# Kernel optimization log

Hardware: AMD Instinct MI355X
Metric: run time of the kernel (lower is better)

## Reference

```python
import math
import jax, jax.numpy as jnp
import numpy as np

N_HEAD = 16
ROPE_BASE = 10000.0


def _rope_tables(T, half, dtype):
    # build_sin_cos(seq_len, dim=head_dim//2): inv freq of length `half`
    pos = jnp.arange(T, dtype=jnp.float32)[:, None]                       # (T,1)
    inv = jnp.exp(jnp.arange(0, 2 * half, 2, dtype=jnp.float32) * (-math.log(ROPE_BASE) / (2 * half)))
    ang = pos * inv                                                        # (T, half)
    return jnp.sin(ang).astype(dtype), jnp.cos(ang).astype(dtype)


def _apply_rope(q, k, sin, cos):
    # q,k: (B,T,H,Dh); sin,cos: (T, Dh//2) -> broadcast over batch and heads
    half = q.shape[-1] // 2
    s = sin[None, :, None, :]
    c = cos[None, :, None, :]
    q1, q2 = q[..., :half], q[..., half:]
    k1, k2 = k[..., :half], k[..., half:]
    q = jnp.concatenate([q1 * c - q2 * s, q2 * c + q1 * s], axis=-1)
    k = jnp.concatenate([k1 * c - k2 * s, k2 * c + k1 * s], axis=-1)
    return q, k


def setup_inputs() -> dict:
    key = jax.random.key(0)
    k1, k2, k3 = jax.random.split(key, 3)
    B, T, C = 2, 2048, 2048
    x = jax.random.normal(k1, (B, T, C), dtype=jnp.float32)
    w_qkv = jax.random.normal(k2, (3 * C, C), dtype=jnp.float32) * (1.0 / math.sqrt(C))
    w_proj = jax.random.normal(k3, (C, C), dtype=jnp.float32) * (1.0 / math.sqrt(C))
    return {"x": x, "w_qkv": w_qkv, "w_proj": w_proj}


def reference(x, w_qkv, w_proj):
    B, T, C = x.shape
    H = N_HEAD
    Dh = C // H
    # fused QKV projection (Linear, no bias): (B,T,3C) -> (B,T,3,H,Dh)
    qkv = jnp.einsum('btc,oc->bto', x, w_qkv).reshape(B, T, 3, H, Dh)
    q, k, v = qkv[:, :, 0], qkv[:, :, 1], qkv[:, :, 2]          # (B,T,H,Dh)
    sin, cos = _rope_tables(T, Dh // 2, x.dtype)
    q, k = _apply_rope(q, k, sin, cos)
    # causal attention, scale 1/sqrt(Dh) (flash default softmax_scale=None)
    scale = 1.0 / math.sqrt(Dh)
    scores = jnp.einsum('bqhd,bkhd->bhqk', q, k) * scale        # (B,H,T,T)
    mask = jnp.tril(jnp.ones((T, T), dtype=bool))
    scores = jnp.where(mask[None, None], scores, jnp.finfo(scores.dtype).min)
    probs = jax.nn.softmax(scores, axis=-1)
    out = jnp.einsum('bhqk,bkhd->bqhd', probs, v)               # (B,T,H,Dh)
    # faithful to original: permute(0,2,1,3) then reshape_as(x)
    out = jnp.transpose(out, (0, 2, 1, 3)).reshape(B, T, C)
    return jnp.einsum('btc,oc->bto', out, w_proj)
```

## Files before the change

### kernel.cpp

```cpp
#include <hip/hip_runtime.h>
#include <hip/hip_bf16.h>

typedef __bf16 bf16_t;
typedef __bf16 bf16x8 __attribute__((ext_vector_type(8)));
typedef float f32x4 __attribute__((ext_vector_type(4)));

#define MFMA16(a, b, c) __builtin_amdgcn_mfma_f32_16x16x32_bf16(a, b, c, 0, 0, 0)

__device__ __forceinline__ void async_copy16(const void* g, void* l) {
  __builtin_amdgcn_global_load_lds(
      (const __attribute__((address_space(1))) void*)g,
      (__attribute__((address_space(3))) void*)l, 16, 0, 0);
}

__global__ void cast_f32_bf16(const float* __restrict__ in, bf16_t* __restrict__ out, int n8) {
  int stride = gridDim.x * blockDim.x;
  for (int i = blockIdx.x * blockDim.x + threadIdx.x; i < n8; i += stride) {
    const float* p = in + (size_t)i * 8;
    f32x4 a = *(const f32x4*)p;
    f32x4 b = *(const f32x4*)(p + 4);
    bf16x8 o;
    o[0] = (bf16_t)a[0]; o[1] = (bf16_t)a[1]; o[2] = (bf16_t)a[2]; o[3] = (bf16_t)a[3];
    o[4] = (bf16_t)b[0]; o[5] = (bf16_t)b[1]; o[6] = (bf16_t)b[2]; o[7] = (bf16_t)b[3];
    *(bf16x8*)(out + (size_t)i * 8) = o;
  }
}

__global__ __launch_bounds__(512, 2) void gemm_qkv(
    const bf16_t* __restrict__ A, const bf16_t* __restrict__ Bw,
    bf16_t* __restrict__ qo, bf16_t* __restrict__ ko,
    int K) {
  __shared__ __align__(16) char lds[131072];
  int tid = threadIdx.x;
  int w = tid >> 6, lane = tid & 63;
  int wm = w & 1, wn = w >> 1;
  int mr = lane & 15, kg = lane >> 4;

  int orig = blockIdx.x;
  int chunk = orig & 7, i = orig >> 3;
  int by = (chunk & 3) * 4 + (i & 3);
  int bx = (chunk >> 2) * 8 + (i >> 2);
  int row0 = by * 256, col0 = bx * 256;

  int lr = tid >> 3, ch = (tid & 7) ^ (lr & 7);
  size_t aoff[4], boff[4];
#pragma unroll
  for (int g = 0; g < 4; ++g) {
    int gr = g * 32 + (lr & 31) + (lr >> 5) * 128;
    aoff[g] = (size_t)(row0 + gr) * K + ch * 8;
  }
#pragma unroll
  for (int p = 0; p < 4; ++p) {
    int gr = (lr >> 4) * 64 + p * 16 + (lr & 15);
    boff[p] = (size_t)(col0 + gr) * K + ch * 8;
  }

  auto stgA = [&](int q, int g, int kt) {
    async_copy16(A + aoff[g] + kt * 64, lds + q * 65536 + g * 8192 + tid * 16);
  };
  auto stgB = [&](int q, int p, int kt) {
    async_copy16(Bw + boff[p] + kt * 64, lds + q * 65536 + 32768 + p * 8192 + tid * 16);
  };

  f32x4 zero = {0.f, 0.f, 0.f, 0.f};
  f32x4 acc[8][4];
#pragma unroll
  for (int mi = 0; mi < 8; ++mi)
#pragma unroll
    for (int ni = 0; ni < 4; ++ni) acc[mi][ni] = zero;

  int nt = K >> 6;

  stgB(0, 0, 0); stgB(0, 1, 0); stgB(0, 2, 0); stgB(0, 3, 0);
  stgA(0, 0, 0); stgA(0, 1, 0); stgA(0, 2, 0); stgA(0, 3, 0);
  asm volatile("s_waitcnt vmcnt(0)" ::: "memory");
  __builtin_amdgcn_sched_barrier(0);
  __builtin_amdgcn_s_barrier();
  __builtin_amdgcn_sched_barrier(0);

#pragma unroll 1
  for (int t = 0; t < nt; ++t) {
    int q = t & 1, qn = q ^ 1;
    int kt = (t + 1 < nt) ? (t + 1) : t;
    const char* Ab = lds + q * 65536;
    const char* Bb = Ab + 32768;
    bf16x8 bf[4][2];

#define QKV_PHASE(MI0, STG0, STG1, WAIT)                                        \
    {                                                                           \
      int r0 = ((MI0) >> 1) * 64 + wm * 32 + mr;                                \
      int r1 = r0 + 16;                                                         \
      bf16x8 a00 = *(const bf16x8*)(Ab + r0 * 128 + ((kg * 16) ^ ((r0 & 7) << 4)));      \
      bf16x8 a01 = *(const bf16x8*)(Ab + r0 * 128 + ((64 + kg * 16) ^ ((r0 & 7) << 4))); \
      bf16x8 a10 = *(const bf16x8*)(Ab + r1 * 128 + ((kg * 16) ^ ((r1 & 7) << 4)));      \
      bf16x8 a11 = *(const bf16x8*)(Ab + r1 * 128 + ((64 + kg * 16) ^ ((r1 & 7) << 4))); \
      STG0; STG1;                                                               \
      __builtin_amdgcn_sched_barrier(0);                                        \
      asm volatile("s_waitcnt vmcnt(" #WAIT ")" ::: "memory");                  \
      __builtin_amdgcn_s_barrier();                                             \
      asm volatile("s_waitcnt lgkmcnt(0)" ::: "memory");                        \
      __builtin_amdgcn_sched_barrier(0);                                        \
      __builtin_amdgcn_s_setprio(1);                                            \
      _Pragma("unroll")                                                         \
      for (int ni = 0; ni < 4; ++ni) {                                          \
        acc[MI0][ni] = MFMA16(a00, bf[ni][0], acc[MI0][ni]);                    \
        acc[MI0][ni] = MFMA16(a01, bf[ni][1], acc[MI0][ni]);                    \
        acc[(MI0) + 1][ni] = MFMA16(a10, bf[ni][0], acc[(MI0) + 1][ni]);        \
        acc[(MI0) + 1][ni] = MFMA16(a11, bf[ni][1], acc[(MI0) + 1][ni]);        \
      }                                                                         \
      __builtin_amdgcn_s_setprio(0);                                            \
      __builtin_amdgcn_sched_barrier(0);                                        \
      __builtin_amdgcn_s_barrier();                                             \
      __builtin_amdgcn_sched_barrier(0);                                        \
    }

#pragma unroll
    for (int ni = 0; ni < 4; ++ni) {
      int rb = ni * 64 + wn * 16 + mr;
      bf[ni][0] = *(const bf16x8*)(Bb + rb * 128 + ((kg * 16) ^ ((rb & 7) << 4)));
      bf[ni][1] = *(const bf16x8*)(Bb + rb * 128 + ((64 + kg * 16) ^ ((rb & 7) << 4)));
    }
    QKV_PHASE(0, stgB(qn, 0, kt), stgB(qn, 1, kt), 4)
    QKV_PHASE(2, stgB(qn, 2, kt), stgB(qn, 3, kt), 5)
    QKV_PHASE(4, stgA(qn, 0, kt), stgA(qn, 1, kt), 6)
    QKV_PHASE(6, stgA(qn, 2, kt), stgA(qn, 3, kt), 3)
#undef QKV_PHASE
  }
  asm volatile("s_waitcnt vmcnt(0)" ::: "memory");
  __syncthreads();

  char* tb = &lds[0];
  int s = col0 >> 11;
  int h0 = (col0 >> 7) & 15;
  int b = row0 >> 11, t0 = row0 & 2047;
#pragma unroll
  for (int mi = 0; mi < 8; ++mi)
#pragma unroll
    for (int ni = 0; ni < 4; ++ni)
#pragma unroll
      for (int jj = 0; jj < 4; ++jj) {
        int rl = wm * 128 + mi * 16 + kg * 4 + jj;
        int cb = (wn * 64 + ni * 16 + mr) * 2;
        *(bf16_t*)(tb + rl * 512 + (cb ^ ((rl & 7) << 4))) = (bf16_t)acc[mi][ni][jj];
      }
  __syncthreads();
  int r = tid >> 1, hs = tid & 1;
  const char* rowb = tb + r * 512;
  int sz = (r & 7) << 4;
  int t = t0 + r;
  bf16_t* dst = (s == 0 ? qo : ko) + ((size_t)((b * 16 + h0 + hs) * 2048 + t)) * 128;
  float tf = (float)t;
  const float cinv = -0.20762050593046014f;
  bf16x8 vin[16];
#pragma unroll
  for (int m = 0; m < 16; ++m)
    vin[m] = *(const bf16x8*)(rowb + ((hs * 256 + m * 16) ^ sz));
#pragma unroll
  for (int m = 0; m < 8; ++m) {
    bf16x8 o1, o2;
#pragma unroll
    for (int e = 0; e < 8; ++e) {
      float ang = tf * exp2f((float)(m * 8 + e) * cinv);
      float sv = __sinf(ang), cv = __cosf(ang);
      float x1 = (float)vin[m][e], x2 = (float)vin[m + 8][e];
      o1[e] = (bf16_t)(x1 * cv - x2 * sv);
      o2[e] = (bf16_t)(x2 * cv + x1 * sv);
    }
    *(bf16x8*)(dst + m * 8) = o1;
    *(bf16x8*)(dst + 64 + m * 8) = o2;
  }
}

template <int MODE>
__global__ __launch_bounds__(512, 2) void gemm256(
    const bf16_t* __restrict__ A, const bf16_t* __restrict__ Bw, float* __restrict__ C,
    bf16_t* __restrict__ vto, int M, int N, int K, int nby, int colbase) {
  __shared__ __align__(16) char lds[147456];
  int tid = threadIdx.x;
  int w = tid >> 6, lane = tid & 63;
  int wm = w >> 1, wn = w & 1;
  int mr = lane & 15, kg = lane >> 4;

  int nwg = gridDim.x;
  int orig = blockIdx.x;
  int wgid = (orig & 7) * (nwg >> 3) + (orig >> 3);
  int by = wgid % nby, bx = wgid / nby;
  int row0 = by * 256, col0 = colbase + bx * 128;

  size_t aoff[4], boff[2];
#pragma unroll
  for (int it = 0; it < 4; ++it) {
    int c = tid + it * 512;
    int r = c >> 3;
    int chs = (c & 7) ^ (r & 7);
    aoff[it] = (size_t)(row0 + r) * K + chs * 8;
  }
#pragma unroll
  for (int it = 0; it < 2; ++it) {
    int c = tid + it * 512;
    int r = c >> 3;
    int chs = (c & 7) ^ (r & 7);
    boff[it] = (size_t)(col0 - colbase + r) * K + chs * 8;
  }

  auto stageA = [&](int buf, int kt, int half) {
    char* Ad = &lds[buf * 49152];
#pragma unroll
    for (int it = half * 2; it < half * 2 + 2; ++it)
      async_copy16(A + aoff[it] + kt * 64, Ad + (tid + it * 512) * 16);
  };
  auto stageB = [&](int buf, int kt) {
    char* Bd = &lds[buf * 49152 + 32768];
#pragma unroll
    for (int it = 0; it < 2; ++it)
      async_copy16(Bw + boff[it] + kt * 64, Bd + (tid + it * 512) * 16);
  };

  f32x4 zero = {0.f, 0.f, 0.f, 0.f};
  f32x4 acc[4][4];
#pragma unroll
  for (int mi = 0; mi < 4; ++mi)
#pragma unroll
    for (int ni = 0; ni < 4; ++ni) acc[mi][ni] = zero;

  int nt = K >> 6;
  stageA(0, 0, 0); stageA(0, 0, 1); stageB(0, 0);
  stageA(1, 1, 0); stageA(1, 1, 1); stageB(1, 1);
  asm volatile("s_waitcnt vmcnt(6)" ::: "memory");
  __builtin_amdgcn_sched_barrier(0);
  __builtin_amdgcn_s_barrier();
  __builtin_amdgcn_sched_barrier(0);

#pragma unroll 1
  for (int t = 0; t < nt; ++t) {
    int cur = t % 3;
    int nxt = (t + 2) % 3;
    int kt2 = (t + 2 < nt) ? (t + 2) : t;
    const char* Ab = &lds[cur * 49152];
    const char* Bb = &lds[cur * 49152 + 32768];
    bf16x8 af[4][2], bfr[4][2];
#pragma unroll
    for (int mi = 0; mi < 4; ++mi) {
      int row = wm * 64 + mi * 16 + mr;
      const char* rb = Ab + row * 128;
      int sz = (row & 7) << 4;
      af[mi][0] = *(const bf16x8*)(rb + ((kg * 16) ^ sz));
      af[mi][1] = *(const bf16x8*)(rb + ((64 + kg * 16) ^ sz));
    }
#pragma unroll
    for (int ni = 0; ni < 4; ++ni) {
      int row = wn * 64 + ni * 16 + mr;
      const char* rb = Bb + row * 128;
      int sz = (row & 7) << 4;
      bfr[ni][0] = *(const bf16x8*)(rb + ((kg * 16) ^ sz));
      bfr[ni][1] = *(const bf16x8*)(rb + ((64 + kg * 16) ^ sz));
    }
    stageA(nxt, kt2, 0);
    __builtin_amdgcn_s_setprio(1);
#pragma unroll
    for (int mi = 0; mi < 4; ++mi) {
      acc[mi][0] = MFMA16(af[mi][0], bfr[0][0], acc[mi][0]);
      acc[mi][0] = MFMA16(af[mi][1], bfr[0][1], acc[mi][0]);
    }
    __builtin_amdgcn_s_setprio(0);
    stageA(nxt, kt2, 1);
    __builtin_amdgcn_s_setprio(1);
#pragma unroll
    for (int mi = 0; mi < 4; ++mi) {
      acc[mi][1] = MFMA16(af[mi][0], bfr[1][0], acc[mi][1]);
      acc[mi][1] = MFMA16(af[mi][1], bfr[1][1], acc[mi][1]);
    }
    __builtin_amdgcn_s_setprio(0);
    stageB(nxt, kt2);
    __builtin_amdgcn_s_setprio(1);
#pragma unroll
    for (int mi = 0; mi < 4; ++mi) {
      acc[mi][2] = MFMA16(af[mi][0], bfr[2][0], acc[mi][2]);
      acc[mi][2] = MFMA16(af[mi][1], bfr[2][1], acc[mi][2]);
      acc[mi][3] = MFMA16(af[mi][0], bfr[3][0], acc[mi][3]);
      acc[mi][3] = MFMA16(af[mi][1], bfr[3][1], acc[mi][3]);
    }
    __builtin_amdgcn_s_setprio(0);
    asm volatile("s_waitcnt vmcnt(6)" ::: "memory");
    __builtin_amdgcn_sched_barrier(0);
    __builtin_amdgcn_s_barrier();
    __builtin_amdgcn_sched_barrier(0);
  }
  asm volatile("s_waitcnt vmcnt(0)" ::: "memory");
  __syncthreads();

  if (MODE == 0) {
#pragma unroll
    for (int mi = 0; mi < 4; ++mi)
#pragma unroll
      for (int ni = 0; ni < 4; ++ni)
#pragma unroll
        for (int jj = 0; jj < 4; ++jj) {
          int row = row0 + wm * 64 + mi * 16 + kg * 4 + jj;
          int col = col0 + wn * 64 + ni * 16 + mr;
          C[(size_t)row * N + col] = acc[mi][ni][jj];
        }
  } else {
    char* tb = &lds[0];
    int h = (col0 >> 7) & 15;
    int b = row0 >> 11, t0 = row0 & 2047;
#pragma unroll
    for (int mi = 0; mi < 4; ++mi)
#pragma unroll
      for (int ni = 0; ni < 4; ++ni)
#pragma unroll
        for (int jj = 0; jj < 4; ++jj) {
          int rloc = wm * 64 + mi * 16 + kg * 4 + jj;
          int cloc = wn * 64 + ni * 16 + mr;
          *(bf16_t*)(tb + cloc * 512 + ((rloc * 2) ^ ((cloc & 7) << 4))) =
              (bf16_t)acc[mi][ni][jj];
        }
    __syncthreads();
    int d = tid >> 2, qt = tid & 3;
    const char* rowb = tb + d * 512;
    int sz = (d & 7) << 4;
    bf16_t* dst = vto + ((size_t)((b * 16 + h) * 128 + d)) * 2048 + t0 + qt * 64;
#pragma unroll
    for (int m2 = 0; m2 < 8; ++m2)
      *(bf16x8*)(dst + m2 * 8) = *(const bf16x8*)(rowb + ((qt * 128 + m2 * 16) ^ sz));
  }
}

__global__ __launch_bounds__(256) void attn_kernel(
    const bf16_t* __restrict__ qg, const bf16_t* __restrict__ kgl,
    const bf16_t* __restrict__ vtg, bf16_t* __restrict__ og) {
  __shared__ __align__(16) bf16_t Ks[2][64 * 128];
  __shared__ __align__(16) bf16_t Vs[2][128 * 64];
  __shared__ __align__(16) bf16_t plds[4][1024];
  const int T = 2048;
  int tid = threadIdx.x;
  int w = tid >> 6, lane = tid & 63;
  int mr = lane & 15, kg = lane >> 4;
  int swz = (mr & 7) << 4;

  int L = blockIdx.y * 16 + blockIdx.x;
  int role = (L & 7) * 64 + (L >> 3);
  int bx = role & 15, bh = role >> 4;

  const bf16_t* Q = qg + (size_t)bh * T * 128;
  const bf16_t* K = kgl + (size_t)bh * T * 128;
  const bf16_t* Vt = vtg + (size_t)bh * 128 * T;

  int sb = tid * 16;
  int krl = sb >> 8;
  int kc = (sb & 255) ^ ((krl & 7) << 4);
  size_t ksrc = (size_t)krl * 128 + (kc >> 1);
  int vdl = sb >> 7;
  int vc = (sb & 127) ^ ((vdl & 7) << 4);
  size_t vsrc = (size_t)vdl * 2048 + (vc >> 1);

  auto stage = [&](int buf, int kb) {
#pragma unroll
    for (int it = 0; it < 4; ++it)
      async_copy16(K + (size_t)(kb + it * 16) * 128 + ksrc, &Ks[buf][it * 2048 + tid * 8]);
#pragma unroll
    for (int it = 0; it < 4; ++it)
      async_copy16(Vt + (size_t)it * 65536 + kb + vsrc, &Vs[buf][it * 2048 + tid * 8]);
  };

  const float cscale = 0.12751744f;
  f32x4 zero = {0.f, 0.f, 0.f, 0.f};
  bf16_t* P = &plds[w][0];
  int b = bh >> 4, h = bh & 15;

#pragma unroll 1
  for (int ph = 0; ph < 2; ++ph) {
    int qb = ph ? bx : (31 - bx);
    int qr0 = qb * 64 + w * 16;
    bf16x8 qf[4];
#pragma unroll
    for (int db = 0; db < 4; ++db)
      qf[db] = *(const bf16x8*)(Q + (size_t)(qr0 + mr) * 128 + db * 32 + kg * 8);

    f32x4 acc[8];
#pragma unroll
    for (int d2 = 0; d2 < 8; ++d2) acc[d2] = zero;
    float mrun[4] = {-1e30f, -1e30f, -1e30f, -1e30f};
    float lpart[4] = {0.f, 0.f, 0.f, 0.f};

    int nj = qb + 1;
    __syncthreads();
    stage(0, 0);
    int cur = 0;
#pragma unroll 1
    for (int j = 0; j < nj; ++j) {
      __syncthreads();
      if (j + 1 < nj) stage(cur ^ 1, (j + 1) * 64);
      const char* KsB = (const char*)&Ks[cur][0];
      const char* VsB = (const char*)&Vs[cur][0];
      int kb = j * 64;
      f32x4 s[4];
      __builtin_amdgcn_s_setprio(1);
#pragma unroll
      for (int ntl = 0; ntl < 4; ++ntl) {
        s[ntl] = zero;
        int rowb = (ntl * 16 + mr) * 256;
#pragma unroll
        for (int db = 0; db < 4; ++db) {
          bf16x8 kf = *(const bf16x8*)(KsB + rowb + ((db * 64 + kg * 16) ^ swz));
          s[ntl] = MFMA16(qf[db], kf, s[ntl]);
        }
      }
      __builtin_amdgcn_s_setprio(0);
      float pvv[4][4];
      float lmax[4] = {-3e38f, -3e38f, -3e38f, -3e38f};
      bool diag = (j == qb);
#pragma unroll
      for (int ntl = 0; ntl < 4; ++ntl)
#pragma unroll
        for (int jj = 0; jj < 4; ++jj) {
          float v = s[ntl][jj] * cscale;
          if (diag && (kb + ntl * 16 + mr) > (qr0 + kg * 4 + jj)) v = -1e30f;
          pvv[ntl][jj] = v;
          lmax[jj] = fmaxf(lmax[jj], v);
        }
      bool ok = true;
#pragma unroll
      for (int jj = 0; jj < 4; ++jj) ok &= (lmax[jj] <= mrun[jj] + 8.0f);
      if (!__all(ok)) {
        float tmax[4];
#pragma unroll
        for (int jj = 0; jj < 4; ++jj) tmax[jj] = lmax[jj];
#pragma unroll
        for (int m = 1; m < 16; m <<= 1)
#pragma unroll
          for (int jj = 0; jj < 4; ++jj)
            tmax[jj] = fmaxf(tmax[jj], __shfl_xor(tmax[jj], m, 64));
#pragma unroll
        for (int jj = 0; jj < 4; ++jj) {
          float mn = fmaxf(mrun[jj], tmax[jj]);
          float corr = __builtin_amdgcn_exp2f(mrun[jj] - mn);
          mrun[jj] = mn;
          lpart[jj] *= corr;
#pragma unroll
          for (int d2 = 0; d2 < 8; ++d2) acc[d2][jj] *= corr;
        }
      }
#pragma unroll
      for (int ntl = 0; ntl < 4; ++ntl)
#pragma unroll
        for (int jj = 0; jj < 4; ++jj) {
          float p = __builtin_amdgcn_exp2f(pvv[ntl][jj] - mrun[jj]);
          pvv[ntl][jj] = p;
          lpart[jj] += p;
        }
#pragma unroll
      for (int ntl = 0; ntl < 4; ++ntl)
#pragma unroll
        for (int jj = 0; jj < 4; ++jj) {
          int rr = kg * 4 + jj;
          int cbyte = (mr + ntl * 16) * 2;
          *(bf16_t*)((char*)P + rr * 128 + (cbyte ^ ((rr & 7) << 4))) = (bf16_t)pvv[ntl][jj];
        }
      __builtin_amdgcn_s_setprio(1);
#pragma unroll
      for (int ks = 0; ks < 2; ++ks) {
        int cb = (ks * 32 + kg * 8) * 2;
        bf16x8 pa = *(const bf16x8*)((const char*)P + mr * 128 + (cb ^ ((mr & 7) << 4)));
#pragma unroll
        for (int d2 = 0; d2 < 8; ++d2) {
          bf16x8 vf = *(const bf16x8*)(VsB + (d2 * 16 + mr) * 128 + ((ks * 64 + kg * 16) ^ swz));
          acc[d2] = MFMA16(pa, vf, acc[d2]);
        }
      }
      __builtin_amdgcn_s_setprio(0);
      cur ^= 1;
    }
#pragma unroll
    for (int m = 1; m < 16; m <<= 1)
#pragma unroll
      for (int jj = 0; jj < 4; ++jj) lpart[jj] += __shfl_xor(lpart[jj], m, 64);
#pragma unroll
    for (int jj = 0; jj < 4; ++jj) {
      float invl = 1.0f / lpart[jj];
      int t = qr0 + kg * 4 + jj;
      size_t row = (size_t)b * 2048 + h * 128 + (t >> 4);
      bf16_t* orow = og + row * 2048 + (t & 15) * 128;
#pragma unroll
      for (int d2 = 0; d2 < 8; ++d2)
        orow[d2 * 16 + mr] = (bf16_t)(acc[d2][jj] * invl);
    }
  }
}

extern "C" void kernel_launch(void* const* d_in, const int* in_sizes, int n_in,
                              void* d_out, int out_size, void* d_ws, size_t ws_size,
                              hipStream_t stream) {
  const float* x = (const float*)d_in[0];
  const float* wqkv = (const float*)d_in[1];
  const float* wproj = (const float*)d_in[2];
  float* out = (float*)d_out;
  char* ws = (char*)d_ws;

  const size_t OFF_WQKV = 16777216;
  const size_t OFF_Q = 41943040;
  const size_t OFF_K = 58720256;
  const size_t OFF_VT = 75497472;

  bf16_t* xb = (bf16_t*)(ws);
  bf16_t* wqkvb = (bf16_t*)(ws + OFF_WQKV);
  bf16_t* g_q = (bf16_t*)(ws + OFF_Q);
  bf16_t* g_k = (bf16_t*)(ws + OFF_K);
  bf16_t* g_vt = (bf16_t*)(ws + OFF_VT);
  bf16_t* g_att = (bf16_t*)(ws);
  bf16_t* wprojb = (bf16_t*)(ws + OFF_WQKV);

  cast_f32_bf16<<<2048, 256, 0, stream>>>(x, xb, 8388608 / 8);
  cast_f32_bf16<<<2048, 256, 0, stream>>>(wqkv, wqkvb, 12582912 / 8);
  gemm_qkv<<<256, 512, 0, stream>>>(xb, wqkvb, g_q, g_k, 2048);
  gemm256<1><<<256, 512, 0, stream>>>(xb, wqkvb + (size_t)4096 * 2048, nullptr, g_vt,
                                      4096, 2048, 2048, 16, 4096);
  cast_f32_bf16<<<2048, 256, 0, stream>>>(wproj, wprojb, 4194304 / 8);
  attn_kernel<<<dim3(16, 32), 256, 0, stream>>>(g_q, g_k, g_vt, g_att);
  gemm256<0><<<256, 512, 0, stream>>>(g_att, wprojb, out, nullptr, 4096, 2048, 2048, 16, 0);
}
```

Measured before the change: 246.4 us.

## Single-buffer attention K/V tiles for higher occupancy and fold softmax scale into Q

The attention kernel moves from double-buffered to single-buffered K/V LDS tiles and adds a launch bound of 4 blocks per CU. Each tile load now waits for completion before compute, trading load/compute overlap for more resident waves. The softmax scale (including log2e) is applied to Q in the RoPE epilogue rather than per score, which removes a multiply per score element but rounds the scaled Q to bf16.

```diff
diff --git a/kernel.cpp b/kernel.cpp
--- a/kernel.cpp
+++ b/kernel.cpp
@@ -151,6 +151,7 @@
   bf16_t* dst = (s == 0 ? qo : ko) + ((size_t)((b * 16 + h0 + hs) * 2048 + t)) * 128;
   float tf = (float)t;
   const float cinv = -0.20762050593046014f;
+  float postm = (s == 0) ? 0.12751744f : 1.0f;
   bf16x8 vin[16];
 #pragma unroll
   for (int m = 0; m < 16; ++m)
@@ -163,8 +164,8 @@
       float ang = tf * exp2f((float)(m * 8 + e) * cinv);
       float sv = __sinf(ang), cv = __cosf(ang);
       float x1 = (float)vin[m][e], x2 = (float)vin[m + 8][e];
-      o1[e] = (bf16_t)(x1 * cv - x2 * sv);
-      o2[e] = (bf16_t)(x2 * cv + x1 * sv);
+      o1[e] = (bf16_t)((x1 * cv - x2 * sv) * postm);
+      o2[e] = (bf16_t)((x2 * cv + x1 * sv) * postm);
     }
     *(bf16x8*)(dst + m * 8) = o1;
     *(bf16x8*)(dst + 64 + m * 8) = o2;
@@ -326,11 +327,11 @@
   }
 }
 
-__global__ __launch_bounds__(256) void attn_kernel(
+__global__ __launch_bounds__(256, 4) void attn_kernel(
     const bf16_t* __restrict__ qg, const bf16_t* __restrict__ kgl,
     const bf16_t* __restrict__ vtg, bf16_t* __restrict__ og) {
-  __shared__ __align__(16) bf16_t Ks[2][64 * 128];
-  __shared__ __align__(16) bf16_t Vs[2][128 * 64];
+  __shared__ __align__(16) bf16_t Ks[64 * 128];
+  __shared__ __align__(16) bf16_t Vs[128 * 64];
   __shared__ __align__(16) bf16_t plds[4][1024];
   const int T = 2048;
   int tid = threadIdx.x;
@@ -354,16 +355,15 @@
   int vc = (sb & 127) ^ ((vdl & 7) << 4);
   size_t vsrc = (size_t)vdl * 2048 + (vc >> 1);
 
-  auto stage = [&](int buf, int kb) {
+  auto stage = [&](int kb) {
 #pragma unroll
     for (int it = 0; it < 4; ++it)
-      async_copy16(K + (size_t)(kb + it * 16) * 128 + ksrc, &Ks[buf][it * 2048 + tid * 8]);
+      async_copy16(K + (size_t)(kb + it * 16) * 128 + ksrc, &Ks[it * 2048 + tid * 8]);
 #pragma unroll
     for (int it = 0; it < 4; ++it)
-      async_copy16(Vt + (size_t)it * 65536 + kb + vsrc, &Vs[buf][it * 2048 + tid * 8]);
+      async_copy16(Vt + (size_t)it * 65536 + kb + vsrc, &Vs[it * 2048 + tid * 8]);
   };
 
-  const float cscale = 0.12751744f;
   f32x4 zero = {0.f, 0.f, 0.f, 0.f};
   bf16_t* P = &plds[w][0];
   int b = bh >> 4, h = bh & 15;
@@ -384,15 +384,15 @@
     float lpart[4] = {0.f, 0.f, 0.f, 0.f};
 
     int nj = qb + 1;
-    __syncthreads();
-    stage(0, 0);
-    int cur = 0;
 #pragma unroll 1
     for (int j = 0; j < nj; ++j) {
       __syncthreads();
-      if (j + 1 < nj) stage(cur ^ 1, (j + 1) * 64);
-      const char* KsB = (const char*)&Ks[cur][0];
-      const char* VsB = (const char*)&Vs[cur][0];
+      stage(j * 64);
+      asm volatile("s_waitcnt vmcnt(0)" ::: "memory");
+      __builtin_amdgcn_sched_barrier(0);
+      __syncthreads();
+      const char* KsB = (const char*)&Ks[0];
+      const char* VsB = (const char*)&Vs[0];
       int kb = j * 64;
       f32x4 s[4];
       __builtin_amdgcn_s_setprio(1);
@@ -414,7 +414,7 @@
       for (int ntl = 0; ntl < 4; ++ntl)
 #pragma unroll
         for (int jj = 0; jj < 4; ++jj) {
-          float v = s[ntl][jj] * cscale;
+          float v = s[ntl][jj];
           if (diag && (kb + ntl * 16 + mr) > (qr0 + kg * 4 + jj)) v = -1e30f;
           pvv[ntl][jj] = v;
           lmax[jj] = fmaxf(lmax[jj], v);
@@ -469,7 +469,6 @@
         }
       }
       __builtin_amdgcn_s_setprio(0);
-      cur ^= 1;
     }
 #pragma unroll
     for (int m = 1; m < 16; m <<= 1)
```

Result: no change. 245.7 us (-0.3%).
